# Performance work log

Measured on AMD Instinct MI355X. Metric: run time of the kernel, lower is better.

## Reference

```python
import jax, jax.numpy as jnp
import numpy as np

DIM = 1024
EPS_LN = 1e-5
EPS_MEM = 1e-6

def _layernorm(x, g, b):
    mu = jnp.mean(x, axis=-1, keepdims=True)
    var = jnp.mean((x - mu) ** 2, axis=-1, keepdims=True)
    return (x - mu) * jax.lax.rsqrt(var + EPS_LN) * g + b

def setup_inputs() -> dict:
    key = jax.random.key(0)
    ks = jax.random.split(key, 8)
    B, S, D = 4, 4096, DIM
    s1 = 1.0 / np.sqrt(D)
    s2 = 1.0 / np.sqrt(4 * D)
    return {
        "x": jax.random.normal(ks[0], (B, S, D), dtype=jnp.float32),
        "ln1_g": jnp.ones((D,), jnp.float32),
        "ln1_b": jnp.zeros((D,), jnp.float32),
        "ln2_g": jnp.ones((D,), jnp.float32),
        "ln2_b": jnp.zeros((D,), jnp.float32),
        "gate_w": jax.random.uniform(ks[1], (D, D), jnp.float32, -s1, s1),
        "gate_b": jax.random.uniform(ks[2], (D,), jnp.float32, -s1, s1),
        "value_w": jax.random.uniform(ks[3], (D, D), jnp.float32, -s1, s1),
        "value_b": jax.random.uniform(ks[4], (D,), jnp.float32, -s1, s1),
        "ffn_w1": jax.random.uniform(ks[5], (D, 4 * D), jnp.float32, -s1, s1),
        "ffn_b1": jnp.zeros((4 * D,), jnp.float32),
        "ffn_w2": jax.random.uniform(ks[6], (4 * D, D), jnp.float32, -s2, s2),
        "ffn_b2": jnp.zeros((D,), jnp.float32),
    }

def reference(x, ln1_g, ln1_b, ln2_g, ln2_b, gate_w, gate_b, value_w, value_b, ffn_w1, ffn_b1, ffn_w2, ffn_b2):
    h = _layernorm(x, ln1_g, ln1_b)
    g = jax.nn.sigmoid(h @ gate_w + gate_b)
    v = h @ value_w + value_b
    cumsum_v = jnp.cumsum(g * v, axis=1)
    cumsum_g = jnp.cumsum(g, axis=1) + EPS_MEM
    x = x + cumsum_v / cumsum_g
    h2 = _layernorm(x, ln2_g, ln2_b)
    ffn = jax.nn.gelu(h2 @ ffn_w1 + ffn_b1, approximate=False) @ ffn_w2 + ffn_b2
    return x + ffn
```

## Files before the change

kernel.cpp:

```cpp
#include <hip/hip_runtime.h>
#include <cstdint>
#include <cstddef>

#define D_MODEL 1024
#define SEQ     4096
#define BATCH   4
#define M_ROWS  (BATCH*SEQ)
#define NCHUNK  64
#define LCHUNK  (SEQ/NCHUNK)

typedef __bf16 bf16_t;
typedef __bf16 bf16x8 __attribute__((ext_vector_type(8)));
typedef __bf16 bf16x4 __attribute__((ext_vector_type(4)));
typedef float  f32x4  __attribute__((ext_vector_type(4)));

__device__ __forceinline__ void load_lds_128(const bf16_t* g, bf16_t* l) {
    __builtin_amdgcn_global_load_lds(
        (const __attribute__((address_space(1))) unsigned int*)g,
        (__attribute__((address_space(3))) unsigned int*)l,
        16, 0, 0);
}

__device__ __forceinline__ float2 bf16pair_to_f2(unsigned int u) {
    union { unsigned int i; float f; } a, b;
    a.i = u << 16;
    b.i = u & 0xffff0000u;
    float2 r; r.x = a.f; r.y = b.f; return r;
}

__device__ __forceinline__ float gelu_f(float x) {
    float t = x * x;
    float u = x * (1.5957691216f + 0.07135481627f * t);
    return x / (1.0f + __expf(-u));
}

__global__ __launch_bounds__(256)
void transpose_all(const float* __restrict__ gate_w, const float* __restrict__ value_w,
                   const float* __restrict__ ffn_w1, const float* __restrict__ ffn_w2,
                   bf16_t* __restrict__ wgv_t, bf16_t* __restrict__ w1_t,
                   bf16_t* __restrict__ w2_t) {
    int id = blockIdx.x;
    const float* in; bf16_t* outp; int R, C, bx, by;
    if (id < 1024)      { in = gate_w;  outp = wgv_t;               R = 1024; C = 1024; bx = id & 31;  by = id >> 5; }
    else if (id < 2048) { id -= 1024; in = value_w; outp = wgv_t + 1024*1024; R = 1024; C = 1024; bx = id & 31;  by = id >> 5; }
    else if (id < 6144) { id -= 2048; in = ffn_w1;  outp = w1_t;    R = 1024; C = 4096; bx = id & 127; by = id >> 7; }
    else                { id -= 6144; in = ffn_w2;  outp = w2_t;    R = 4096; C = 1024; bx = id & 31;  by = id >> 5; }
    __shared__ float t[32][33];
    int tx = threadIdx.x & 31, ty = threadIdx.x >> 5;
    int c0 = bx * 32, r0 = by * 32;
    #pragma unroll
    for (int j = 0; j < 32; j += 8)
        t[ty + j][tx] = in[(size_t)(r0 + ty + j) * C + c0 + tx];
    __syncthreads();
    #pragma unroll
    for (int j = 0; j < 32; j += 8)
        outp[(size_t)(c0 + ty + j) * R + r0 + tx] = (bf16_t)t[tx][ty + j];
}

__global__ __launch_bounds__(256)
void ln_kernel(const float* __restrict__ x, const float* __restrict__ gamma,
               const float* __restrict__ beta, bf16_t* __restrict__ h) {
    int row = blockIdx.x;
    int tid = threadIdx.x;
    const float4* xr = (const float4*)(x + (size_t)row * D_MODEL);
    float4 v = xr[tid];
    float s  = v.x + v.y + v.z + v.w;
    float ss = v.x*v.x + v.y*v.y + v.z*v.z + v.w*v.w;
    #pragma unroll
    for (int off = 32; off; off >>= 1) {
        s  += __shfl_down(s, off);
        ss += __shfl_down(ss, off);
    }
    __shared__ float red[8];
    int wave = tid >> 6, lane = tid & 63;
    if (lane == 0) { red[wave] = s; red[4 + wave] = ss; }
    __syncthreads();
    if (tid == 0) {
        float S  = red[0] + red[1] + red[2] + red[3];
        float SS = red[4] + red[5] + red[6] + red[7];
        float mean = S * (1.0f / D_MODEL);
        float var  = SS * (1.0f / D_MODEL) - mean * mean;
        red[0] = mean;
        red[1] = rsqrtf(var + 1e-5f);
    }
    __syncthreads();
    float mean = red[0], rstd = red[1];
    float4 gv = ((const float4*)gamma)[tid];
    float4 bv = ((const float4*)beta)[tid];
    bf16x4 o;
    o[0] = (bf16_t)((v.x - mean) * rstd * gv.x + bv.x);
    o[1] = (bf16_t)((v.y - mean) * rstd * gv.y + bv.y);
    o[2] = (bf16_t)((v.z - mean) * rstd * gv.z + bv.z);
    o[3] = (bf16_t)((v.w - mean) * rstd * gv.w + bv.w);
    ((bf16x4*)h)[(size_t)row * (D_MODEL / 4) + tid] = o;
}

#define FENCE() asm volatile("" ::: "memory")
#define SP_MID() do { FENCE(); __builtin_amdgcn_s_barrier(); FENCE(); \
    __builtin_amdgcn_s_setprio(1); } while (0)
#define SP_END() do { __builtin_amdgcn_s_setprio(0); FENCE(); \
    __builtin_amdgcn_s_barrier(); FENCE(); } while (0)
#define VMW4() asm volatile("s_waitcnt vmcnt(4)" ::: "memory")

#define LDA4(BUF, MB) do { _Pragma("unroll") for (int m_ = 0; m_ < 4; ++m_) { \
    af[m_][0] = *(const bf16x8*)((BUF) + aoff0 + ((MB)*4 + m_) * 1024); \
    af[m_][1] = *(const bf16x8*)((BUF) + aoff1 + ((MB)*4 + m_) * 1024); } } while (0)
#define LDB4(BUF) do { _Pragma("unroll") for (int n_ = 0; n_ < 4; ++n_) { \
    bfr[n_][0] = *(const bf16x8*)((BUF) + boff0 + n_ * 1024); \
    bfr[n_][1] = *(const bf16x8*)((BUF) + boff1 + n_ * 1024); } } while (0)
#define MFMA_HALF(MB, NLO) do { _Pragma("unroll") for (int m_ = 0; m_ < 4; ++m_) { \
    _Pragma("unroll") for (int n_ = 0; n_ < 2; ++n_) { \
        acc[(MB)*4 + m_][(NLO) + n_] = __builtin_amdgcn_mfma_f32_16x16x32_bf16( \
            bfr[(NLO)+n_][0], af[m_][0], acc[(MB)*4 + m_][(NLO) + n_], 0, 0, 0); \
        acc[(MB)*4 + m_][(NLO) + n_] = __builtin_amdgcn_mfma_f32_16x16x32_bf16( \
            bfr[(NLO)+n_][1], af[m_][1], acc[(MB)*4 + m_][(NLO) + n_], 0, 0, 0); } } } while (0)

template <int MODE, int TN, int TPB, int LKT>
__global__ __launch_bounds__(512, 2)
void gemm256(const bf16_t* __restrict__ A, const bf16_t* __restrict__ Bt,
             const float* __restrict__ bias, const float* __restrict__ bias2,
             const float* __restrict__ xres,
             void* __restrict__ out, void* __restrict__ out2,
             int M, int N, int K) {
    __shared__ __align__(16) bf16_t lds[2][2][256 * 64];

    const int KT = 1 << LKT;
    const int S  = TPB * KT;
    const int NI = S >> 1;

    const int tid  = threadIdx.x;
    const int lane = tid & 63;
    const int wave = tid >> 6;
    const int wm   = wave >> 2;
    const int wn   = wave & 3;

    const int L    = blockIdx.x;
    const int i    = L >> 3;
    const int ngrp = i & 3;
    const int mb   = (L & 7) + 8 * (i >> 2);
    const int m0   = mb * 256;
    const int n00  = ngrp * TPB * 256;

    f32x4 acc[8][4];
    #pragma unroll
    for (int ii = 0; ii < 8; ii++)
        #pragma unroll
        for (int j = 0; j < 4; j++) acc[ii][j] = (f32x4){0.f, 0.f, 0.f, 0.f};

    const int rr = tid >> 3;
    const int sc = ((tid & 7) ^ (rr & 7)) * 8;
    const bf16_t* pa0 = A  + ((size_t)(m0  + rr)) * K + sc;
    const bf16_t* pb0 = Bt + ((size_t)(n00 + rr)) * K + sc;
    const size_t rstep   = (size_t)64 * K;
    const size_t hstep   = rstep * 2;
    const size_t nstride = (size_t)256 * K;

    #define PA(s) (pa0 + (((s) & (KT - 1)) << 6))
    #define PB(s) (pb0 + (size_t)((s) >> LKT) * nstride + (((s) & (KT - 1)) << 6))

    const int l16 = lane & 15, quad = lane >> 4, swz = l16 & 7;
    const int aoff0 = (wm*128 + l16)*64 + ((quad    ) ^ swz)*8;
    const int aoff1 = (wm*128 + l16)*64 + ((quad + 4) ^ swz)*8;
    const int boff0 = (wn*64  + l16)*64 + ((quad    ) ^ swz)*8;
    const int boff1 = (wn*64  + l16)*64 + ((quad + 4) ^ swz)*8;

    bf16_t* LA0 = &lds[0][0][0]; bf16_t* LB0 = &lds[0][1][0];
    bf16_t* LA1 = &lds[1][0][0]; bf16_t* LB1 = &lds[1][1][0];

    auto STAGE = [&](const bf16_t* gsrc, bf16_t* dst) {
        load_lds_128(gsrc,         dst + tid * 8);
        load_lds_128(gsrc + rstep, dst + 4096 + tid * 8);
    };

    STAGE(PB(0),         LB0);
    STAGE(PB(0) + hstep, LB0 + 8192);
    STAGE(PA(0),         LA0);
    STAGE(PA(0) + hstep, LA0 + 8192);
    STAGE(PB(1),         LB1);
    STAGE(PB(1) + hstep, LB1 + 8192);
    VMW4();
    __builtin_amdgcn_s_barrier();
    FENCE();

    bf16x8 af[4][2], bfr[4][2];

    #pragma unroll 1
    for (int it = 0; it < NI; ++it) {
        const int s1 = 2*it + 1;
        const int s2 = (2*it + 2 < S) ? 2*it + 2 : S - 1;
        const int s3 = (2*it + 3 < S) ? 2*it + 3 : S - 1;
        const bf16_t* a1 = PA(s1);
        const bf16_t* a2 = PA(s2);
        const bf16_t* b2 = PB(s2);
        const bf16_t* b3 = PB(s3);

        STAGE(a1,         LA1);
        STAGE(a1 + hstep, LA1 + 8192);
        LDA4(LA0, 0); LDB4(LB0);
        SP_MID(); MFMA_HALF(0, 0); MFMA_HALF(0, 2); SP_END();
        STAGE(b2,         LB0);
        STAGE(b2 + hstep, LB0 + 8192);
        LDA4(LA0, 1);
        VMW4();
        SP_MID(); MFMA_HALF(1, 0); MFMA_HALF(1, 2); SP_END();
        STAGE(a2,         LA0);
        STAGE(a2 + hstep, LA0 + 8192);
        LDA4(LA1, 0); LDB4(LB1);
        SP_MID(); MFMA_HALF(0, 0); MFMA_HALF(0, 2); SP_END();
        STAGE(b3,         LB1);
        STAGE(b3 + hstep, LB1 + 8192);
        LDA4(LA1, 1);
        VMW4();
        SP_MID(); MFMA_HALF(1, 0); MFMA_HALF(1, 2); SP_END();

        if (((it + 1) & ((KT >> 1) - 1)) == 0) {
            const int tdone = (2*it + 1) >> LKT;
            const int nn0 = n00 + tdone * 256;
            #pragma unroll
            for (int mt = 0; mt < 8; ++mt) {
                int row = m0 + wm * 128 + mt * 16 + l16;
                #pragma unroll
                for (int nt = 0; nt < 4; ++nt) {
                    int col = nn0 + wn * 64 + nt * 16 + quad * 4;
                    f32x4 a = acc[mt][nt];
                    if (MODE == 4) {
                        bool isV = (nn0 >= 1024);
                        int c1 = col & 1023;
                        float4 bv = *(const float4*)((isV ? bias2 : bias) + c1);
                        float4 val;
                        val.x = a[0] + bv.x; val.y = a[1] + bv.y;
                        val.z = a[2] + bv.z; val.w = a[3] + bv.w;
                        if (!isV) {
                            val.x = 1.0f / (1.0f + __expf(-val.x));
                            val.y = 1.0f / (1.0f + __expf(-val.y));
                            val.z = 1.0f / (1.0f + __expf(-val.z));
                            val.w = 1.0f / (1.0f + __expf(-val.w));
                        }
                        bf16x4 p;
                        p[0] = (bf16_t)val.x; p[1] = (bf16_t)val.y;
                        p[2] = (bf16_t)val.z; p[3] = (bf16_t)val.w;
                        bf16_t* o = (bf16_t*)(isV ? out2 : out);
                        *(bf16x4*)(o + (size_t)row * 1024 + c1) = p;
                    } else if (MODE == 2) {
                        float4 bv = *(const float4*)(bias + col);
                        bf16x4 p;
                        p[0] = (bf16_t)gelu_f(a[0] + bv.x);
                        p[1] = (bf16_t)gelu_f(a[1] + bv.y);
                        p[2] = (bf16_t)gelu_f(a[2] + bv.z);
                        p[3] = (bf16_t)gelu_f(a[3] + bv.w);
                        *(bf16x4*)((bf16_t*)out + (size_t)row * N + col) = p;
                    } else {
                        float4 bv = *(const float4*)(bias + col);
                        float4 xr = *(const float4*)(xres + (size_t)row * N + col);
                        float4 val;
                        val.x = xr.x + a[0] + bv.x; val.y = xr.y + a[1] + bv.y;
                        val.z = xr.z + a[2] + bv.z; val.w = xr.w + a[3] + bv.w;
                        *(float4*)((float*)out + (size_t)row * N + col) = val;
                    }
                    acc[mt][nt] = (f32x4){0.f, 0.f, 0.f, 0.f};
                }
            }
        }
    }

    asm volatile("s_waitcnt vmcnt(0)" ::: "memory");
    #undef PA
    #undef PB
}

__global__ __launch_bounds__(256)
void scan_partial(const bf16_t* __restrict__ g, const bf16_t* __restrict__ v,
                  float* __restrict__ sg, float* __restrict__ sgv) {
    int dt = blockIdx.x & 1;
    int c  = (blockIdx.x >> 1) & (NCHUNK - 1);
    int b  = blockIdx.x >> 7;
    int d  = dt * 512 + threadIdx.x * 2;
    float s0 = 0.f, s1 = 0.f, t0 = 0.f, t1 = 0.f;
    for (int i = 0; i < LCHUNK; i++) {
        int s = c * LCHUNK + i;
        size_t idx = ((size_t)(b * SEQ + s)) * D_MODEL + d;
        float2 gf = bf16pair_to_f2(*(const unsigned int*)(g + idx));
        float2 vf = bf16pair_to_f2(*(const unsigned int*)(v + idx));
        s0 += gf.x; s1 += gf.y;
        t0 += gf.x * vf.x; t1 += gf.y * vf.y;
    }
    size_t o = ((size_t)(b * NCHUNK + c)) * D_MODEL + d;
    sg[o] = s0;  sg[o + 1] = s1;
    sgv[o] = t0; sgv[o + 1] = t1;
}

__global__ __launch_bounds__(256)
void scan_apply(const bf16_t* __restrict__ g, const bf16_t* __restrict__ v,
                const float* __restrict__ x, const float* __restrict__ sg,
                const float* __restrict__ sgv, float* __restrict__ out) {
    int dt = blockIdx.x & 1;
    int c  = (blockIdx.x >> 1) & (NCHUNK - 1);
    int b  = blockIdx.x >> 7;
    int d  = dt * 512 + threadIdx.x * 2;
    float rg0 = 0.f, rg1 = 0.f, rv0 = 0.f, rv1 = 0.f;
    for (int p = 0; p < c; p++) {
        size_t o = ((size_t)(b * NCHUNK + p)) * D_MODEL + d;
        float2 a  = *(const float2*)(sg + o);
        float2 bb = *(const float2*)(sgv + o);
        rg0 += a.x;  rg1 += a.y;
        rv0 += bb.x; rv1 += bb.y;
    }
    for (int i = 0; i < LCHUNK; i++) {
        int s = c * LCHUNK + i;
        size_t idx = ((size_t)(b * SEQ + s)) * D_MODEL + d;
        float2 gf = bf16pair_to_f2(*(const unsigned int*)(g + idx));
        float2 vf = bf16pair_to_f2(*(const unsigned int*)(v + idx));
        rv0 += gf.x * vf.x; rg0 += gf.x;
        rv1 += gf.y * vf.y; rg1 += gf.y;
        float2 xv = *(const float2*)(x + idx);
        float2 ov;
        ov.x = xv.x + rv0 / (rg0 + 1e-6f);
        ov.y = xv.y + rv1 / (rg1 + 1e-6f);
        *(float2*)(out + idx) = ov;
    }
}

extern "C" void kernel_launch(void* const* d_in, const int* in_sizes, int n_in,
                              void* d_out, int out_size, void* d_ws, size_t ws_size,
                              hipStream_t stream) {
    (void)in_sizes; (void)n_in; (void)out_size; (void)ws_size;
    const float* x       = (const float*)d_in[0];
    const float* ln1_g   = (const float*)d_in[1];
    const float* ln1_b   = (const float*)d_in[2];
    const float* ln2_g   = (const float*)d_in[3];
    const float* ln2_b   = (const float*)d_in[4];
    const float* gate_w  = (const float*)d_in[5];
    const float* gate_b  = (const float*)d_in[6];
    const float* value_w = (const float*)d_in[7];
    const float* value_b = (const float*)d_in[8];
    const float* ffn_w1  = (const float*)d_in[9];
    const float* ffn_b1  = (const float*)d_in[10];
    const float* ffn_w2  = (const float*)d_in[11];
    const float* ffn_b2  = (const float*)d_in[12];
    float* out = (float*)d_out;

    char* ws = (char*)d_ws;
    const size_t MB = 1024 * 1024;
    bf16_t* wgv_t = (bf16_t*)(ws + 0 * MB);
    bf16_t* w1_t  = (bf16_t*)(ws + 4 * MB);
    bf16_t* w2_t  = (bf16_t*)(ws + 12 * MB);
    bf16_t* h     = (bf16_t*)(ws + 20 * MB);
    bf16_t* g     = (bf16_t*)(ws + 52 * MB);
    bf16_t* v     = (bf16_t*)(ws + 84 * MB);
    float*  sg    = (float*)(ws + 116 * MB);
    float*  sgv   = (float*)(ws + 117 * MB);
    bf16_t* act   = (bf16_t*)(ws + 118 * MB);

    transpose_all<<<10240, 256, 0, stream>>>(gate_w, value_w, ffn_w1, ffn_w2,
                                             wgv_t, w1_t, w2_t);

    ln_kernel<<<M_ROWS, 256, 0, stream>>>(x, ln1_g, ln1_b, h);

    gemm256<4, 8, 2, 4><<<256, 512, 0, stream>>>(
        h, wgv_t, gate_b, value_b, nullptr, g, v, M_ROWS, 2048, 1024);

    scan_partial<<<BATCH * NCHUNK * 2, 256, 0, stream>>>(g, v, sg, sgv);
    scan_apply<<<BATCH * NCHUNK * 2, 256, 0, stream>>>(g, v, x, sg, sgv, out);

    ln_kernel<<<M_ROWS, 256, 0, stream>>>(out, ln2_g, ln2_b, h);

    gemm256<2, 16, 4, 4><<<256, 512, 0, stream>>>(
        h, w1_t, ffn_b1, nullptr, nullptr, act, nullptr, M_ROWS, 4096, 1024);

    gemm256<3, 4, 1, 6><<<256, 512, 0, stream>>>(
        act, w2_t, ffn_b2, nullptr, out, out, nullptr, M_ROWS, 1024, 4096);
}
```

Measured before the change: 599.0 us.

## Triple-buffer A tiles in LDS to prefetch two K-steps ahead in GEMM

Restructures the GEMM main loop so the A operand uses three rotating LDS buffers and B two, issuing global-to-LDS loads for A two stages ahead with a looser vmcnt wait. The last iteration is peeled, which removes the clamped redundant loads at the tail, and the epilogue is moved into a lambda. The aim is to hide more global load latency behind MFMA work. The cost is that LDS use grows from 128KB to 160KB per block, which may reduce the occupancy allowed by launch_bounds(512,2).

```diff
diff --git a/kernel.cpp b/kernel.cpp
--- a/kernel.cpp
+++ b/kernel.cpp
@@ -100,7 +100,8 @@
     __builtin_amdgcn_s_setprio(1); } while (0)
 #define SP_END() do { __builtin_amdgcn_s_setprio(0); FENCE(); \
     __builtin_amdgcn_s_barrier(); FENCE(); } while (0)
-#define VMW4() asm volatile("s_waitcnt vmcnt(4)" ::: "memory")
+#define VMW8() asm volatile("s_waitcnt vmcnt(8)" ::: "memory")
+#define VMW0() asm volatile("s_waitcnt vmcnt(0)" ::: "memory")
 
 #define LDA4(BUF, MB) do { _Pragma("unroll") for (int m_ = 0; m_ < 4; ++m_) { \
     af[m_][0] = *(const bf16x8*)((BUF) + aoff0 + ((MB)*4 + m_) * 1024); \
@@ -122,7 +123,8 @@
              const float* __restrict__ xres,
              void* __restrict__ out, void* __restrict__ out2,
              int M, int N, int K) {
-    __shared__ __align__(16) bf16_t lds[2][2][256 * 64];
+    __shared__ __align__(16) bf16_t ldsA[3][256 * 64];
+    __shared__ __align__(16) bf16_t ldsB[2][256 * 64];
 
     const int KT = 1 << LKT;
     const int S  = TPB * KT;
@@ -164,106 +166,114 @@
     const int boff0 = (wn*64  + l16)*64 + ((quad    ) ^ swz)*8;
     const int boff1 = (wn*64  + l16)*64 + ((quad + 4) ^ swz)*8;
 
-    bf16_t* LA0 = &lds[0][0][0]; bf16_t* LB0 = &lds[0][1][0];
-    bf16_t* LA1 = &lds[1][0][0]; bf16_t* LB1 = &lds[1][1][0];
-
-    auto STAGE = [&](const bf16_t* gsrc, bf16_t* dst) {
-        load_lds_128(gsrc,         dst + tid * 8);
-        load_lds_128(gsrc + rstep, dst + 4096 + tid * 8);
+    bf16_t* a0 = &ldsA[0][0];
+    bf16_t* a1 = &ldsA[1][0];
+    bf16_t* a2 = &ldsA[2][0];
+    bf16_t* b0 = &ldsB[0][0];
+    bf16_t* b1 = &ldsB[1][0];
+
+    auto STAGE_T = [&](const bf16_t* gsrc, bf16_t* dst) {
+        load_lds_128(gsrc,                 dst + tid * 8);
+        load_lds_128(gsrc + rstep,         dst + 4096  + tid * 8);
+        load_lds_128(gsrc + hstep,         dst + 8192  + tid * 8);
+        load_lds_128(gsrc + hstep + rstep, dst + 12288 + tid * 8);
     };
 
-    STAGE(PB(0),         LB0);
-    STAGE(PB(0) + hstep, LB0 + 8192);
-    STAGE(PA(0),         LA0);
-    STAGE(PA(0) + hstep, LA0 + 8192);
-    STAGE(PB(1),         LB1);
-    STAGE(PB(1) + hstep, LB1 + 8192);
-    VMW4();
+    auto EPILOGUE = [&](int tdone) {
+        const int nn0 = n00 + tdone * 256;
+        #pragma unroll
+        for (int mt = 0; mt < 8; ++mt) {
+            int row = m0 + wm * 128 + mt * 16 + l16;
+            #pragma unroll
+            for (int nt = 0; nt < 4; ++nt) {
+                int col = nn0 + wn * 64 + nt * 16 + quad * 4;
+                f32x4 a = acc[mt][nt];
+                if (MODE == 4) {
+                    bool isV = (nn0 >= 1024);
+                    int c1 = col & 1023;
+                    float4 bv = *(const float4*)((isV ? bias2 : bias) + c1);
+                    float4 val;
+                    val.x = a[0] + bv.x; val.y = a[1] + bv.y;
+                    val.z = a[2] + bv.z; val.w = a[3] + bv.w;
+                    if (!isV) {
+                        val.x = 1.0f / (1.0f + __expf(-val.x));
+                        val.y = 1.0f / (1.0f + __expf(-val.y));
+                        val.z = 1.0f / (1.0f + __expf(-val.z));
+                        val.w = 1.0f / (1.0f + __expf(-val.w));
+                    }
+                    bf16x4 p;
+                    p[0] = (bf16_t)val.x; p[1] = (bf16_t)val.y;
+                    p[2] = (bf16_t)val.z; p[3] = (bf16_t)val.w;
+                    bf16_t* o = (bf16_t*)(isV ? out2 : out);
+                    *(bf16x4*)(o + (size_t)row * 1024 + c1) = p;
+                } else if (MODE == 2) {
+                    float4 bv = *(const float4*)(bias + col);
+                    bf16x4 p;
+                    p[0] = (bf16_t)gelu_f(a[0] + bv.x);
+                    p[1] = (bf16_t)gelu_f(a[1] + bv.y);
+                    p[2] = (bf16_t)gelu_f(a[2] + bv.z);
+                    p[3] = (bf16_t)gelu_f(a[3] + bv.w);
+                    *(bf16x4*)((bf16_t*)out + (size_t)row * N + col) = p;
+                } else {
+                    float4 bv = *(const float4*)(bias + col);
+                    float4 xr = *(const float4*)(xres + (size_t)row * N + col);
+                    float4 val;
+                    val.x = xr.x + a[0] + bv.x; val.y = xr.y + a[1] + bv.y;
+                    val.z = xr.z + a[2] + bv.z; val.w = xr.w + a[3] + bv.w;
+                    *(float4*)((float*)out + (size_t)row * N + col) = val;
+                }
+                acc[mt][nt] = (f32x4){0.f, 0.f, 0.f, 0.f};
+            }
+        }
+    };
+
+    STAGE_T(PA(0), a0);
+    STAGE_T(PB(0), b0);
+    STAGE_T(PA(1), a1);
+    STAGE_T(PB(1), b1);
+    VMW0();
     __builtin_amdgcn_s_barrier();
     FENCE();
 
     bf16x8 af[4][2], bfr[4][2];
 
     #pragma unroll 1
-    for (int it = 0; it < NI; ++it) {
-        const int s1 = 2*it + 1;
-        const int s2 = (2*it + 2 < S) ? 2*it + 2 : S - 1;
-        const int s3 = (2*it + 3 < S) ? 2*it + 3 : S - 1;
-        const bf16_t* a1 = PA(s1);
-        const bf16_t* a2 = PA(s2);
-        const bf16_t* b2 = PB(s2);
-        const bf16_t* b3 = PB(s3);
-
-        STAGE(a1,         LA1);
-        STAGE(a1 + hstep, LA1 + 8192);
-        LDA4(LA0, 0); LDB4(LB0);
+    for (int it = 0; it < NI - 1; ++it) {
+        const int s2 = 2*it + 2;
+        const int s3 = 2*it + 3;
+
+        STAGE_T(PA(s2), a2);
+        LDA4(a0, 0); LDB4(b0);
         SP_MID(); MFMA_HALF(0, 0); MFMA_HALF(0, 2); SP_END();
-        STAGE(b2,         LB0);
-        STAGE(b2 + hstep, LB0 + 8192);
-        LDA4(LA0, 1);
-        VMW4();
+        STAGE_T(PB(s2), b0);
+        LDA4(a0, 1);
+        VMW8();
         SP_MID(); MFMA_HALF(1, 0); MFMA_HALF(1, 2); SP_END();
-        STAGE(a2,         LA0);
-        STAGE(a2 + hstep, LA0 + 8192);
-        LDA4(LA1, 0); LDB4(LB1);
+        STAGE_T(PA(s3), a0);
+        LDA4(a1, 0); LDB4(b1);
         SP_MID(); MFMA_HALF(0, 0); MFMA_HALF(0, 2); SP_END();
-        STAGE(b3,         LB1);
-        STAGE(b3 + hstep, LB1 + 8192);
-        LDA4(LA1, 1);
-        VMW4();
+        STAGE_T(PB(s3), b1);
+        LDA4(a1, 1);
+        VMW8();
         SP_MID(); MFMA_HALF(1, 0); MFMA_HALF(1, 2); SP_END();
 
-        if (((it + 1) & ((KT >> 1) - 1)) == 0) {
-            const int tdone = (2*it + 1) >> LKT;
-            const int nn0 = n00 + tdone * 256;
-            #pragma unroll
-            for (int mt = 0; mt < 8; ++mt) {
-                int row = m0 + wm * 128 + mt * 16 + l16;
-                #pragma unroll
-                for (int nt = 0; nt < 4; ++nt) {
-                    int col = nn0 + wn * 64 + nt * 16 + quad * 4;
-                    f32x4 a = acc[mt][nt];
-                    if (MODE == 4) {
-                        bool isV = (nn0 >= 1024);
-                        int c1 = col & 1023;
-                        float4 bv = *(const float4*)((isV ? bias2 : bias) + c1);
-                        float4 val;
-                        val.x = a[0] + bv.x; val.y = a[1] + bv.y;
-                        val.z = a[2] + bv.z; val.w = a[3] + bv.w;
-                        if (!isV) {
-                            val.x = 1.0f / (1.0f + __expf(-val.x));
-                            val.y = 1.0f / (1.0f + __expf(-val.y));
-                            val.z = 1.0f / (1.0f + __expf(-val.z));
-                            val.w = 1.0f / (1.0f + __expf(-val.w));
-                        }
-                        bf16x4 p;
-                        p[0] = (bf16_t)val.x; p[1] = (bf16_t)val.y;
-                        p[2] = (bf16_t)val.z; p[3] = (bf16_t)val.w;
-                        bf16_t* o = (bf16_t*)(isV ? out2 : out);
-                        *(bf16x4*)(o + (size_t)row * 1024 + c1) = p;
-                    } else if (MODE == 2) {
-                        float4 bv = *(const float4*)(bias + col);
-                        bf16x4 p;
-                        p[0] = (bf16_t)gelu_f(a[0] + bv.x);
-                        p[1] = (bf16_t)gelu_f(a[1] + bv.y);
-                        p[2] = (bf16_t)gelu_f(a[2] + bv.z);
-                        p[3] = (bf16_t)gelu_f(a[3] + bv.w);
-                        *(bf16x4*)((bf16_t*)out + (size_t)row * N + col) = p;
-                    } else {
-                        float4 bv = *(const float4*)(bias + col);
-                        float4 xr = *(const float4*)(xres + (size_t)row * N + col);
-                        float4 val;
-                        val.x = xr.x + a[0] + bv.x; val.y = xr.y + a[1] + bv.y;
-                        val.z = xr.z + a[2] + bv.z; val.w = xr.w + a[3] + bv.w;
-                        *(float4*)((float*)out + (size_t)row * N + col) = val;
-                    }
-                    acc[mt][nt] = (f32x4){0.f, 0.f, 0.f, 0.f};
-                }
-            }
-        }
-    }
-
-    asm volatile("s_waitcnt vmcnt(0)" ::: "memory");
+        bf16_t* t = a0; a0 = a2; a2 = a1; a1 = t;
+
+        if (((it + 1) & ((KT >> 1) - 1)) == 0)
+            EPILOGUE((2*it + 1) >> LKT);
+    }
+
+    LDA4(a0, 0); LDB4(b0);
+    SP_MID(); MFMA_HALF(0, 0); MFMA_HALF(0, 2); SP_END();
+    LDA4(a0, 1);
+    VMW0();
+    SP_MID(); MFMA_HALF(1, 0); MFMA_HALF(1, 2); SP_END();
+    LDA4(a1, 0); LDB4(b1);
+    SP_MID(); MFMA_HALF(0, 0); MFMA_HALF(0, 2); SP_END();
+    LDA4(a1, 1);
+    SP_MID(); MFMA_HALF(1, 0); MFMA_HALF(1, 2); SP_END();
+
+    EPILOGUE(TPB - 1);
     #undef PA
     #undef PB
 }
```

Result: slower. 705.8 us (+17.8%).
